# Performance work log

Measured on AMD Instinct MI355X. Metric: run time of the kernel, lower is better.

## Reference

```python
import jax, jax.numpy as jnp
import numpy as np

B, T, DIN, DH, A = 2048, 32, 1024, 64, 64
EPS = 1e-12  # tf.contrib.layers.layer_norm variance epsilon


def _ln(x, g, b, axes):
    mu = jnp.mean(x, axes, keepdims=True)
    var = jnp.var(x, axes, keepdims=True)
    return (x - mu) / jnp.sqrt(var + EPS) * g + b


def _lstm(x_seq, W, b, H):
    # BasicLSTMCell: z = [x, h] @ W + b ; gates in order i, j, f, o ; forget_bias=1.0
    def step(carry, xt):
        c, h = carry
        z = jnp.concatenate([xt, h], axis=-1) @ W + b
        i, j, f, o = jnp.split(z, 4, axis=-1)
        c = c * jax.nn.sigmoid(f + 1.0) + jax.nn.sigmoid(i) * jnp.tanh(j)
        h = jnp.tanh(c) * jax.nn.sigmoid(o)
        return (c, h), h
    Bb = x_seq.shape[0]
    init = (jnp.zeros((Bb, H), x_seq.dtype), jnp.zeros((Bb, H), x_seq.dtype))
    _, hs = jax.lax.scan(step, init, jnp.swapaxes(x_seq, 0, 1))  # [T,B,H]
    return jnp.swapaxes(hs, 0, 1)  # [B,T,H]


def _revseq(x, lens):
    # tf.reverse_sequence along time axis 1
    t = jnp.arange(x.shape[1])[None, :]
    idx = jnp.where(t < lens[:, None], lens[:, None] - 1 - t, t)
    return jnp.take_along_axis(x, idx[:, :, None], axis=1)


def setup_inputs() -> dict:
    key = jax.random.key(0)
    ks = jax.random.split(key, 8)
    H = 512
    s_d = 1.0 / np.sqrt(DIN)
    s_l = 1.0 / np.sqrt(DH + H)
    return {
        "ud": jax.random.normal(ks[0], (B * T, DIN), jnp.float32),
        "mask": jnp.ones((B, T), jnp.float32),
        "au": jax.random.randint(ks[1], (B,), 1, T + 1, jnp.int32),
        "n_hidden": H,
        "ln1_g": jnp.ones((DIN,), jnp.float32),
        "ln1_b": jnp.zeros((DIN,), jnp.float32),
        "W_dense": jax.random.normal(ks[2], (DIN, DH), jnp.float32) * s_d,
        "b_dense": jnp.zeros((DH,), jnp.float32),
        "ln2_g": jnp.ones((DH,), jnp.float32),
        "ln2_b": jnp.zeros((DH,), jnp.float32),
        "W_fw": jax.random.normal(ks[3], (DH + H, 4 * H), jnp.float32) * s_l,
        "b_fw": jnp.zeros((4 * H,), jnp.float32),
        "W_bw": jax.random.normal(ks[4], (DH + H, 4 * H), jnp.float32) * s_l,
        "b_bw": jnp.zeros((4 * H,), jnp.float32),
        "ln3_g": jnp.ones((2 * H,), jnp.float32),
        "ln3_b": jnp.zeros((2 * H,), jnp.float32),
        "W_conv": jax.random.uniform(ks[5], (2 * H, A), jnp.float32, -0.003, 0.003),
        "b_conv": jnp.zeros((A,), jnp.float32),
    }


def reference(ud, mask, au, n_hidden, ln1_g, ln1_b, W_dense, b_dense, ln2_g, ln2_b,
              W_fw, b_fw, W_bw, b_bw, ln3_g, ln3_b, W_conv, b_conv):
    H = n_hidden
    x = _ln(ud, ln1_g, ln1_b, -1)                     # [B*T, DIN]
    x = x @ W_dense + b_dense                          # [B*T, DH]
    x = jax.nn.relu(_ln(x, ln2_g, ln2_b, -1))
    x = x.reshape(B, T, DH)
    tmask = (jnp.arange(T)[None, :] < au[:, None]).astype(x.dtype)  # [B,T]
    fw = _lstm(x, W_fw, b_fw, H) * tmask[:, :, None]
    bw = _revseq(_lstm(_revseq(x, au), W_bw, b_bw, H) * tmask[:, :, None], au)
    h = jnp.concatenate([fw, bw], axis=-1)             # [B,T,2H]
    # contrib layer_norm: begin_norm_axis=1 -> normalize over (T, 2H) jointly
    h = jax.nn.relu(_ln(h, ln3_g, ln3_b, (1, 2)))
    # conv1d kernel_size=stride=2H on [B, T*2H, 1] == per-timestep matmul
    out = jnp.tanh(jnp.einsum('bth,ha->bta', h, W_conv) + b_conv)  # [B,T,A]
    return out
```

## Files before the change

### kernel.cpp

```cpp
#include <hip/hip_runtime.h>

#define B_   2048
#define T_   32
#define DIN_ 1024
#define DH_  64
#define H_   512
#define KL_  576
#define AO_  64

typedef unsigned short u16;
typedef unsigned int   u32;
typedef __attribute__((ext_vector_type(8))) short          bf16x8;
typedef __attribute__((ext_vector_type(8))) unsigned short u16x8;
typedef __attribute__((ext_vector_type(4))) float          f32x4;

__device__ __forceinline__ u16 f2bf(float f) {
  u32 u = __builtin_bit_cast(u32, f);
  u = (u + 0x7FFFu + ((u >> 16) & 1u)) >> 16;
  return (u16)u;
}
__device__ __forceinline__ float bf2f(u16 s) {
  return __builtin_bit_cast(float, (u32)s << 16);
}
__device__ __forceinline__ float sigm(float x) { return 1.f / (1.f + __expf(-x)); }
__device__ __forceinline__ float tanh_(float x) { return 1.f - 2.f / (__expf(2.f * x) + 1.f); }

__device__ __forceinline__ void gl_lds16(const void* g, void* l) {
  __builtin_amdgcn_global_load_lds((const __attribute__((address_space(1))) u32*)g,
                                   (__attribute__((address_space(3))) u32*)l, 16, 0, 0);
}

__global__ __launch_bounds__(256) void k_transpose(const float* __restrict__ src,
                                                   u16* __restrict__ dst, int K, int N) {
  __shared__ float t[32][33];
  const int n0 = blockIdx.x * 32, k0 = blockIdx.y * 32;
  const int a = threadIdx.x >> 5, b = threadIdx.x & 31;
#pragma unroll
  for (int i = 0; i < 4; ++i)
    t[a + 8 * i][b] = src[(size_t)(k0 + a + 8 * i) * N + n0 + b];
  __syncthreads();
#pragma unroll
  for (int i = 0; i < 4; ++i)
    dst[(size_t)(n0 + a + 8 * i) * K + k0 + b] = f2bf(t[b][a + 8 * i]);
}

__global__ void k_gw(const float* __restrict__ W, const float* __restrict__ g,
                     const float* __restrict__ b, float* __restrict__ gW,
                     float* __restrict__ bW) {
  const int n = threadIdx.x;
  float sg = 0.f, sb = 0.f;
  for (int k = 0; k < DIN_; ++k) {
    const float w = W[k * DH_ + n];
    sg += g[k] * w; sb += b[k] * w;
  }
  gW[n] = sg; bW[n] = sb;
}

__global__ __launch_bounds__(256) void k_front(
    const float* __restrict__ ud, const float* __restrict__ g1,
    const u16* __restrict__ Wdt, const float* __restrict__ gW,
    const float* __restrict__ bW, const float* __restrict__ bd,
    const float* __restrict__ g2, const float* __restrict__ b2,
    u16* __restrict__ xout) {
  __shared__ u16 lA[64 * 32];
  __shared__ u16 lB[64 * 32];
  __shared__ float smu[64], srs[64];
  const int tid = threadIdx.x, wave = tid >> 6, lane = tid & 63;
  const int m0 = blockIdx.x * 64;
  const int arow = tid >> 2, ach = tid & 3;
  const float* __restrict__ udp = ud + (size_t)(m0 + arow) * DIN_ + ach * 8;
  const float* __restrict__ g1p = g1 + ach * 8;
  const int cB = wave * 16 + (lane >> 2);
  const u16* __restrict__ wdp = Wdt + (size_t)cB * DIN_ + (lane & 3) * 8;
  u16* const lBb = &lB[wave * 512];
  u16x8* const lAp = (u16x8*)&lA[arow * 32 + ach * 8];
  const int quad = lane >> 4, col = lane & 15;

  float sx = 0.f, sxx = 0.f;
  f32x4 acc[4] = {};
  for (int kt = 0; kt < 32; ++kt) {
    const int k0 = kt * 32;
    __syncthreads();
    const float4 v0 = *(const float4*)(udp + k0);
    const float4 v1 = *(const float4*)(udp + k0 + 4);
    const float4 ga = *(const float4*)(g1p + k0);
    const float4 gb = *(const float4*)(g1p + k0 + 4);
    sx  += v0.x + v0.y + v0.z + v0.w + v1.x + v1.y + v1.z + v1.w;
    sxx += v0.x * v0.x + v0.y * v0.y + v0.z * v0.z + v0.w * v0.w
         + v1.x * v1.x + v1.y * v1.y + v1.z * v1.z + v1.w * v1.w;
    u16x8 pk;
    pk[0] = f2bf(v0.x * ga.x); pk[1] = f2bf(v0.y * ga.y);
    pk[2] = f2bf(v0.z * ga.z); pk[3] = f2bf(v0.w * ga.w);
    pk[4] = f2bf(v1.x * gb.x); pk[5] = f2bf(v1.y * gb.y);
    pk[6] = f2bf(v1.z * gb.z); pk[7] = f2bf(v1.w * gb.w);
    *lAp = pk;
    gl_lds16(wdp + k0, lBb);
    __syncthreads();
    const bf16x8 af = *(const bf16x8*)&lA[(wave * 16 + col) * 32 + quad * 8];
#pragma unroll
    for (int nt = 0; nt < 4; ++nt) {
      const bf16x8 bfr = *(const bf16x8*)&lB[(nt * 16 + col) * 32 + quad * 8];
      acc[nt] = __builtin_amdgcn_mfma_f32_16x16x32_bf16(af, bfr, acc[nt], 0, 0, 0);
    }
  }
  sx  += __shfl_xor(sx, 1);  sx  += __shfl_xor(sx, 2);
  sxx += __shfl_xor(sxx, 1); sxx += __shfl_xor(sxx, 2);
  if ((lane & 3) == 0) {
    const float mu = sx * (1.f / DIN_);
    const float var = sxx * (1.f / DIN_) - mu * mu;
    smu[arow] = mu;
    srs[arow] = rsqrtf(var + 1e-12f);
  }
  __syncthreads();
  float gwv[4], bwv[4], g2v[4], b2v[4];
#pragma unroll
  for (int nt = 0; nt < 4; ++nt) {
    const int n = nt * 16 + col;
    gwv[nt] = gW[n]; bwv[nt] = bW[n] + bd[n]; g2v[nt] = g2[n]; b2v[nt] = b2[n];
  }
#pragma unroll
  for (int r = 0; r < 4; ++r) {
    const int rl = wave * 16 + quad * 4 + r;
    const float mu = smu[rl], rs = srs[rl];
    float y[4]; float s1 = 0.f, s2 = 0.f;
#pragma unroll
    for (int nt = 0; nt < 4; ++nt) {
      y[nt] = rs * (acc[nt][r] - mu * gwv[nt]) + bwv[nt];
      s1 += y[nt]; s2 += y[nt] * y[nt];
    }
    s1 += __shfl_xor(s1, 1); s1 += __shfl_xor(s1, 2);
    s1 += __shfl_xor(s1, 4); s1 += __shfl_xor(s1, 8);
    s2 += __shfl_xor(s2, 1); s2 += __shfl_xor(s2, 2);
    s2 += __shfl_xor(s2, 4); s2 += __shfl_xor(s2, 8);
    const float mu2 = s1 * (1.f / 64.f);
    const float rs2 = rsqrtf(s2 * (1.f / 64.f) - mu2 * mu2 + 1e-12f);
    const size_t R = m0 + rl;
#pragma unroll
    for (int nt = 0; nt < 4; ++nt) {
      const float v = fmaxf((y[nt] - mu2) * rs2 * g2v[nt] + b2v[nt], 0.f);
      xout[R * 64 + nt * 16 + col] = f2bf(v);
    }
  }
}

__global__ __launch_bounds__(256) void k_step(
    const int s, const u16* __restrict__ x, const u16* __restrict__ Wt,
    const float* __restrict__ bfw, const float* __restrict__ bbw,
    const int* __restrict__ au, u16* __restrict__ hstate,
    float* __restrict__ cstate, u16* __restrict__ hout) {
  __shared__ u16 lA[128 * 32];
  __shared__ u16 lB[128 * 32];
  const int tid = threadIdx.x, wave = tid >> 6, lane = tid & 63;
  const int dir = blockIdx.z;
  const int m0 = blockIdx.x * 128;
  const int u0 = blockIdx.y * 32;
  const int rb = s & 1, wb = rb ^ 1;
  const u16* __restrict__ Wtd = Wt + (size_t)dir * 2048 * KL_;
  const float* __restrict__ bias = dir ? bbw : bfw;

  const u16* gx[2]; const u16* gh[2]; const u16* gB[2];
  u16* lab[2]; u16* lbb[2];
#pragma unroll
  for (int i = 0; i < 2; ++i) {
    const int ch = 2 * wave + i;
    const int rl = ch * 16 + (lane >> 2);
    const int b  = m0 + rl;
    const int aub = au[b];
    const int tin = (dir == 0) ? s : ((s < aub) ? (aub - 1 - s) : s);
    gx[i] = x + ((size_t)b * T_ + tin) * DH_ + (lane & 3) * 8;
    gh[i] = hstate + (((size_t)dir * 2 + rb) * B_ + b) * H_ + (lane & 3) * 8;
    const int n = 512 * (ch & 3) + u0 + ((ch >> 2) << 4) + (lane >> 2);
    gB[i] = Wtd + (size_t)n * KL_ + (lane & 3) * 8;
    lab[i] = &lA[ch * 512];
    lbb[i] = &lB[ch * 512];
  }

  f32x4 acc[4][4] = {};
  const int wm = wave >> 1, wn = wave & 1, quad = lane >> 4, col = lane & 15;

  for (int kt = 0; kt < 18; ++kt) {
    const int k0 = kt * 32;
    __syncthreads();
    if (kt < 2) {
      gl_lds16(gx[0] + k0, lab[0]);
      gl_lds16(gx[1] + k0, lab[1]);
    } else {
      gl_lds16(gh[0] + (k0 - 64), lab[0]);
      gl_lds16(gh[1] + (k0 - 64), lab[1]);
    }
    gl_lds16(gB[0] + k0, lbb[0]);
    gl_lds16(gB[1] + k0, lbb[1]);
    __syncthreads();
    bf16x8 bfrag[4];
#pragma unroll
    for (int nt = 0; nt < 4; ++nt)
      bfrag[nt] = *(const bf16x8*)&lB[(wn * 64 + nt * 16 + col) * 32 + quad * 8];
#pragma unroll
    for (int mt = 0; mt < 4; ++mt) {
      const bf16x8 afrag = *(const bf16x8*)&lA[(wm * 64 + mt * 16 + col) * 32 + quad * 8];
#pragma unroll
      for (int nt = 0; nt < 4; ++nt)
        acc[mt][nt] = __builtin_amdgcn_mfma_f32_16x16x32_bf16(afrag, bfrag[nt], acc[mt][nt], 0, 0, 0);
    }
  }

  const int u = u0 + wn * 16 + col;
  const float bi = bias[u], bj = bias[512 + u], bff = bias[1024 + u], bo = bias[1536 + u];
#pragma unroll
  for (int mt = 0; mt < 4; ++mt) {
#pragma unroll
    for (int r = 0; r < 4; ++r) {
      const int brow = m0 + wm * 64 + mt * 16 + quad * 4 + r;
      const size_t ci = ((size_t)dir * B_ + brow) * H_ + u;
      const float zi = acc[mt][0][r] + bi;
      const float zj = acc[mt][1][r] + bj;
      const float zf = acc[mt][2][r] + bff;
      const float zo = acc[mt][3][r] + bo;
      const float cn = cstate[ci] * sigm(zf + 1.f) + sigm(zi) * tanh_(zj);
      const float hn = tanh_(cn) * sigm(zo);
      cstate[ci] = cn;
      hstate[(((size_t)dir * 2 + wb) * B_ + brow) * H_ + u] = f2bf(hn);
      const int aub = au[brow];
      const bool valid = (s < aub);
      const int pos = (dir == 0) ? s : (valid ? (aub - 1 - s) : s);
      const float val = valid ? hn : 0.f;
      hout[((size_t)brow * T_ + pos) * 1024 + (dir ? 512 : 0) + u] = f2bf(val);
    }
  }
}

__global__ __launch_bounds__(256) void k_ln3stats(const u16* __restrict__ hout,
                                                  float* __restrict__ st) {
  const int b = blockIdx.x, tid = threadIdx.x;
  const uint4* __restrict__ p = (const uint4*)(hout + (size_t)b * T_ * 1024);
  float sx = 0.f, sxx = 0.f;
  for (int j = tid; j < 4096; j += 256) {
    const uint4 q = p[j];
    const u32 w[4] = {q.x, q.y, q.z, q.w};
#pragma unroll
    for (int e = 0; e < 4; ++e) {
      const float a = bf2f((u16)(w[e] & 0xffff));
      const float c = bf2f((u16)(w[e] >> 16));
      sx += a + c; sxx += a * a + c * c;
    }
  }
#pragma unroll
  for (int m = 1; m < 64; m <<= 1) { sx += __shfl_xor(sx, m); sxx += __shfl_xor(sxx, m); }
  __shared__ float rs_[4], rq_[4];
  if ((tid & 63) == 0) { rs_[tid >> 6] = sx; rq_[tid >> 6] = sxx; }
  __syncthreads();
  if (tid == 0) {
    const float a = rs_[0] + rs_[1] + rs_[2] + rs_[3];
    const float c = rq_[0] + rq_[1] + rq_[2] + rq_[3];
    const float mu = a / 32768.f;
    const float var = c / 32768.f - mu * mu;
    st[b * 2] = mu; st[b * 2 + 1] = rsqrtf(var + 1e-12f);
  }
}

__global__ __launch_bounds__(256) void k_final(
    const u16* __restrict__ hin, const float* __restrict__ st,
    const float* __restrict__ g3, const float* __restrict__ b3,
    const u16* __restrict__ Wct, const float* __restrict__ bc,
    float* __restrict__ out) {
  __shared__ u16 lA[64 * 32];
  __shared__ u16 lB[64 * 32];
  const int tid = threadIdx.x, wave = tid >> 6, lane = tid & 63;
  const int m0 = blockIdx.x * 64;
  const int arow = tid >> 2, ach = tid & 3;
  const size_t R = m0 + arow;
  const float mu = st[(R >> 5) * 2], rs = st[(R >> 5) * 2 + 1];
  const u16* __restrict__ hp = hin + R * 1024 + ach * 8;
  const float* __restrict__ g3p = g3 + ach * 8;
  const float* __restrict__ b3p = b3 + ach * 8;
  const int cB = wave * 16 + (lane >> 2);
  const u16* __restrict__ wcp = Wct + (size_t)cB * DIN_ + (lane & 3) * 8;
  u16* const lBb = &lB[wave * 512];
  u16x8* const lAp = (u16x8*)&lA[arow * 32 + ach * 8];
  const int quad = lane >> 4, col = lane & 15;
  f32x4 acc[4] = {};
  for (int kt = 0; kt < 32; ++kt) {
    const int k0 = kt * 32;
    __syncthreads();
    const uint4 q = *(const uint4*)(hp + k0);
    const float4 ga = *(const float4*)(g3p + k0);
    const float4 gb = *(const float4*)(g3p + k0 + 4);
    const float4 ba = *(const float4*)(b3p + k0);
    const float4 bb = *(const float4*)(b3p + k0 + 4);
    float hv[8];
    hv[0] = bf2f((u16)(q.x & 0xffff)); hv[1] = bf2f((u16)(q.x >> 16));
    hv[2] = bf2f((u16)(q.y & 0xffff)); hv[3] = bf2f((u16)(q.y >> 16));
    hv[4] = bf2f((u16)(q.z & 0xffff)); hv[5] = bf2f((u16)(q.z >> 16));
    hv[6] = bf2f((u16)(q.w & 0xffff)); hv[7] = bf2f((u16)(q.w >> 16));
    u16x8 pk;
    pk[0] = f2bf(fmaxf((hv[0] - mu) * rs * ga.x + ba.x, 0.f));
    pk[1] = f2bf(fmaxf((hv[1] - mu) * rs * ga.y + ba.y, 0.f));
    pk[2] = f2bf(fmaxf((hv[2] - mu) * rs * ga.z + ba.z, 0.f));
    pk[3] = f2bf(fmaxf((hv[3] - mu) * rs * ga.w + ba.w, 0.f));
    pk[4] = f2bf(fmaxf((hv[4] - mu) * rs * gb.x + bb.x, 0.f));
    pk[5] = f2bf(fmaxf((hv[5] - mu) * rs * gb.y + bb.y, 0.f));
    pk[6] = f2bf(fmaxf((hv[6] - mu) * rs * gb.z + bb.z, 0.f));
    pk[7] = f2bf(fmaxf((hv[7] - mu) * rs * gb.w + bb.w, 0.f));
    *lAp = pk;
    gl_lds16(wcp + k0, lBb);
    __syncthreads();
    const bf16x8 af = *(const bf16x8*)&lA[(wave * 16 + col) * 32 + quad * 8];
#pragma unroll
    for (int nt = 0; nt < 4; ++nt) {
      const bf16x8 bfr = *(const bf16x8*)&lB[(nt * 16 + col) * 32 + quad * 8];
      acc[nt] = __builtin_amdgcn_mfma_f32_16x16x32_bf16(af, bfr, acc[nt], 0, 0, 0);
    }
  }
  float bcv[4];
#pragma unroll
  for (int nt = 0; nt < 4; ++nt) bcv[nt] = bc[nt * 16 + col];
#pragma unroll
  for (int r = 0; r < 4; ++r) {
    const size_t R2 = m0 + wave * 16 + quad * 4 + r;
#pragma unroll
    for (int nt = 0; nt < 4; ++nt)
      out[R2 * 64 + nt * 16 + col] = tanh_(acc[nt][r] + bcv[nt]);
  }
}

extern "C" void kernel_launch(void* const* d_in, const int* in_sizes, int n_in,
                              void* d_out, int out_size, void* d_ws, size_t ws_size,
                              hipStream_t stream) {
  (void)in_sizes; (void)n_in; (void)out_size; (void)ws_size;
  const float* ud  = (const float*)d_in[0];
  const int*   au  = (const int*)d_in[2];
  const float* g1  = (const float*)d_in[4];
  const float* b1  = (const float*)d_in[5];
  const float* Wd  = (const float*)d_in[6];
  const float* bd  = (const float*)d_in[7];
  const float* g2  = (const float*)d_in[8];
  const float* b2  = (const float*)d_in[9];
  const float* Wfw = (const float*)d_in[10];
  const float* bfw = (const float*)d_in[11];
  const float* Wbw = (const float*)d_in[12];
  const float* bbw = (const float*)d_in[13];
  const float* g3  = (const float*)d_in[14];
  const float* b3  = (const float*)d_in[15];
  const float* Wc  = (const float*)d_in[16];
  const float* bc  = (const float*)d_in[17];

  char* p = (char*)d_ws;
  size_t off = 0;
  auto take = [&](size_t bytes) {
    char* r = p + off;
    off = (off + bytes + 255) & ~(size_t)255;
    return r;
  };
  u16*   xbf    = (u16*)  take((size_t)B_ * T_ * DH_ * 2);
  u16*   Wt     = (u16*)  take((size_t)2 * 2048 * KL_ * 2);
  u16*   Wdt    = (u16*)  take((size_t)DH_ * DIN_ * 2);
  u16*   Wct    = (u16*)  take((size_t)AO_ * DIN_ * 2);
  float* gWv    = (float*)take(64 * 4);
  float* bWv    = (float*)take(64 * 4);
  u16*   hstate = (u16*)  take((size_t)2 * 2 * B_ * H_ * 2);
  float* cstate = (float*)take((size_t)2 * B_ * H_ * 4);
  u16*   hout   = (u16*)  take((size_t)B_ * T_ * 1024 * 2);
  float* st3    = (float*)take((size_t)B_ * 2 * 4);

  hipMemsetAsync(hstate, 0, (size_t)2 * 2 * B_ * H_ * 2 + (size_t)2 * B_ * H_ * 4, stream);

  k_transpose<<<dim3(64, 18), 256, 0, stream>>>(Wfw, Wt,              KL_, 2048);
  k_transpose<<<dim3(64, 18), 256, 0, stream>>>(Wbw, Wt + 2048 * KL_, KL_, 2048);
  k_transpose<<<dim3(2, 32),  256, 0, stream>>>(Wd,  Wdt, DIN_, DH_);
  k_transpose<<<dim3(2, 32),  256, 0, stream>>>(Wc,  Wct, DIN_, AO_);
  k_gw<<<1, 64, 0, stream>>>(Wd, g1, b1, gWv, bWv);
  k_front<<<B_ * T_ / 64, 256, 0, stream>>>(ud, g1, Wdt, gWv, bWv, bd, g2, b2, xbf);
  for (int s = 0; s < T_; ++s)
    k_step<<<dim3(16, 16, 2), 256, 0, stream>>>(s, xbf, Wt, bfw, bbw, au, hstate, cstate, hout);
  k_ln3stats<<<B_, 256, 0, stream>>>(hout, st3);
  k_final<<<B_ * T_ / 64, 256, 0, stream>>>(hout, st3, g3, b3, Wct, bc, (float*)d_out);
}
```

Measured before the change: 1.294 ms.

## Double-buffer LSTM step GEMM with K=64 tiles and XOR-swizzled LDS

Reworks the per-timestep LSTM GEMM kernel to use 64-wide K tiles in two LDS buffers. The next tile's global-to-LDS load is issued before the current tile's MFMAs, so there is one barrier per iteration instead of two and fewer iterations. LDS rows are XOR-swizzled to cut bank conflicts on fragment reads. In exchange it uses four times the LDS, which may lower occupancy.

```diff
diff --git a/kernel.cpp b/kernel.cpp
--- a/kernel.cpp
+++ b/kernel.cpp
@@ -148,8 +148,8 @@
     const float* __restrict__ bfw, const float* __restrict__ bbw,
     const int* __restrict__ au, u16* __restrict__ hstate,
     float* __restrict__ cstate, u16* __restrict__ hout) {
-  __shared__ u16 lA[128 * 32];
-  __shared__ u16 lB[128 * 32];
+  __shared__ u16 lA[2][128 * 64];
+  __shared__ u16 lB[2][128 * 64];
   const int tid = threadIdx.x, wave = tid >> 6, lane = tid & 63;
   const int dir = blockIdx.z;
   const int m0 = blockIdx.x * 128;
@@ -158,50 +158,74 @@
   const u16* __restrict__ Wtd = Wt + (size_t)dir * 2048 * KL_;
   const float* __restrict__ bias = dir ? bbw : bfw;
 
-  const u16* gx[2]; const u16* gh[2]; const u16* gB[2];
-  u16* lab[2]; u16* lbb[2];
+  const int lrow = lane >> 3;
+  const int kk = ((lane & 7) ^ lrow) * 8;
+  const int ch0 = 2 * wave, ch1 = ch0 + 1;
+
+  const u16* gx[4]; const u16* gh[2]; const u16* gB[2];
 #pragma unroll
   for (int i = 0; i < 2; ++i) {
-    const int ch = 2 * wave + i;
-    const int rl = ch * 16 + (lane >> 2);
-    const int b  = m0 + rl;
-    const int aub = au[b];
-    const int tin = (dir == 0) ? s : ((s < aub) ? (aub - 1 - s) : s);
-    gx[i] = x + ((size_t)b * T_ + tin) * DH_ + (lane & 3) * 8;
-    gh[i] = hstate + (((size_t)dir * 2 + rb) * B_ + b) * H_ + (lane & 3) * 8;
-    const int n = 512 * (ch & 3) + u0 + ((ch >> 2) << 4) + (lane >> 2);
-    gB[i] = Wtd + (size_t)n * KL_ + (lane & 3) * 8;
-    lab[i] = &lA[ch * 512];
-    lbb[i] = &lB[ch * 512];
-  }
+    const int ch = ch0 + i;
+#pragma unroll
+    for (int h = 0; h < 2; ++h) {
+      const int b = m0 + ch * 16 + h * 8 + lrow;
+      const int aub = au[b];
+      const int tin = (dir == 0) ? s : ((s < aub) ? (aub - 1 - s) : s);
+      gx[i * 2 + h] = x + ((size_t)b * T_ + tin) * DH_ + kk;
+    }
+    const int b0 = m0 + ch * 16 + lrow;
+    gh[i] = hstate + (((size_t)dir * 2 + rb) * B_ + b0) * H_ + kk;
+    const int n = 512 * (ch & 3) + u0 + ((ch >> 2) << 4) + lrow;
+    gB[i] = Wtd + (size_t)n * KL_ + kk;
+  }
+
+  gl_lds16(gx[0], &lA[0][ch0 * 1024]);
+  gl_lds16(gx[1], &lA[0][ch0 * 1024 + 512]);
+  gl_lds16(gx[2], &lA[0][ch1 * 1024]);
+  gl_lds16(gx[3], &lA[0][ch1 * 1024 + 512]);
+  gl_lds16(gB[0],           &lB[0][ch0 * 1024]);
+  gl_lds16(gB[0] + 8 * KL_, &lB[0][ch0 * 1024 + 512]);
+  gl_lds16(gB[1],           &lB[0][ch1 * 1024]);
+  gl_lds16(gB[1] + 8 * KL_, &lB[0][ch1 * 1024 + 512]);
+  __syncthreads();
 
   f32x4 acc[4][4] = {};
   const int wm = wave >> 1, wn = wave & 1, quad = lane >> 4, col = lane & 15;
-
-  for (int kt = 0; kt < 18; ++kt) {
-    const int k0 = kt * 32;
+  const int swz = (col & 7) << 4;
+
+  int cur = 0;
+  for (int kt = 0; kt < 9; ++kt) {
+    if (kt < 8) {
+      const int nb = cur ^ 1;
+      const int kh = kt * 64;
+      gl_lds16(gh[0] + kh,          &lA[nb][ch0 * 1024]);
+      gl_lds16(gh[0] + kh + 8 * H_, &lA[nb][ch0 * 1024 + 512]);
+      gl_lds16(gh[1] + kh,          &lA[nb][ch1 * 1024]);
+      gl_lds16(gh[1] + kh + 8 * H_, &lA[nb][ch1 * 1024 + 512]);
+      gl_lds16(gB[0] + kh + 64,            &lB[nb][ch0 * 1024]);
+      gl_lds16(gB[0] + kh + 64 + 8 * KL_,  &lB[nb][ch0 * 1024 + 512]);
+      gl_lds16(gB[1] + kh + 64,            &lB[nb][ch1 * 1024]);
+      gl_lds16(gB[1] + kh + 64 + 8 * KL_,  &lB[nb][ch1 * 1024 + 512]);
+    }
+    const char* la = (const char*)&lA[cur][0];
+    const char* lb = (const char*)&lB[cur][0];
+#pragma unroll
+    for (int ks = 0; ks < 2; ++ks) {
+      const int bko = (ks * 64 + quad * 16) ^ swz;
+      bf16x8 bfrag[4];
+#pragma unroll
+      for (int nt = 0; nt < 4; ++nt)
+        bfrag[nt] = *(const bf16x8*)(lb + (wn * 64 + nt * 16 + col) * 128 + bko);
+#pragma unroll
+      for (int mt = 0; mt < 4; ++mt) {
+        const bf16x8 afrag = *(const bf16x8*)(la + (wm * 64 + mt * 16 + col) * 128 + bko);
+#pragma unroll
+        for (int nt = 0; nt < 4; ++nt)
+          acc[mt][nt] = __builtin_amdgcn_mfma_f32_16x16x32_bf16(afrag, bfrag[nt], acc[mt][nt], 0, 0, 0);
+      }
+    }
     __syncthreads();
-    if (kt < 2) {
-      gl_lds16(gx[0] + k0, lab[0]);
-      gl_lds16(gx[1] + k0, lab[1]);
-    } else {
-      gl_lds16(gh[0] + (k0 - 64), lab[0]);
-      gl_lds16(gh[1] + (k0 - 64), lab[1]);
-    }
-    gl_lds16(gB[0] + k0, lbb[0]);
-    gl_lds16(gB[1] + k0, lbb[1]);
-    __syncthreads();
-    bf16x8 bfrag[4];
-#pragma unroll
-    for (int nt = 0; nt < 4; ++nt)
-      bfrag[nt] = *(const bf16x8*)&lB[(wn * 64 + nt * 16 + col) * 32 + quad * 8];
-#pragma unroll
-    for (int mt = 0; mt < 4; ++mt) {
-      const bf16x8 afrag = *(const bf16x8*)&lA[(wm * 64 + mt * 16 + col) * 32 + quad * 8];
-#pragma unroll
-      for (int nt = 0; nt < 4; ++nt)
-        acc[mt][nt] = __builtin_amdgcn_mfma_f32_16x16x32_bf16(afrag, bfrag[nt], acc[mt][nt], 0, 0, 0);
-    }
+    cur ^= 1;
   }
 
   const int u = u0 + wn * 16 + col;
```

New measurement: 1.234 ms. 1.05x faster.
